# Performance work log

Hardware: AMD Instinct MI355X
Metric: run time of the kernel (lower is better)

Reference implementation:

```python
import jax, jax.numpy as jnp
import numpy as np

B, VN, LN = 32, 576, 128
V_DIM, L_DIM, E, H = 1024, 768, 1024, 16
D = E // H
SCALE = H ** -0.5  # note: original scales by num_heads**-0.5, NOT head_dim**-0.5


def _xavier(key, shape):
    fan_in, fan_out = shape[1], shape[0]
    lim = np.sqrt(6.0 / (fan_in + fan_out))
    return jax.random.uniform(key, shape, jnp.float32, -lim, lim)


def setup_inputs() -> dict:
    key = jax.random.key(0)
    ks = jax.random.split(key, 10)
    return {
        "v": jax.random.normal(ks[0], (B, VN, V_DIM), jnp.float32),
        "l": jax.random.normal(ks[1], (B, LN, L_DIM), jnp.float32),
        "attention_mask_l": jnp.zeros((LN,), jnp.float32),
        "Wvq": _xavier(ks[2], (E, V_DIM)), "bvq": jnp.zeros((E,), jnp.float32),
        "Wlk": _xavier(ks[3], (E, L_DIM)), "blk": jnp.zeros((E,), jnp.float32),
        "Wvv": _xavier(ks[4], (E, V_DIM)), "bvv": jnp.zeros((E,), jnp.float32),
        "Wlv": _xavier(ks[5], (E, L_DIM)), "blv": jnp.zeros((E,), jnp.float32),
        "Wvo": _xavier(ks[6], (V_DIM, E)), "bvo": jnp.zeros((V_DIM,), jnp.float32),
        "Wlo": _xavier(ks[7], (L_DIM, E)), "blo": jnp.zeros((L_DIM,), jnp.float32),
    }


def reference(v, l, attention_mask_l, Wvq, bvq, Wlk, blk, Wvv, bvv, Wlv, blv, Wvo, bvo, Wlo, blo):
    # mode='vl'; dropout is identity (eval mode)
    q = (v @ Wvq.T + bvq).reshape(B, VN, H, D)          # vision queries
    k = (l @ Wlk.T + blk).reshape(B, LN, H, D)          # language keys
    vv = (v @ Wvv.T + bvv).reshape(B, VN, H, D)         # vision values
    lv = (l @ Wlv.T + blv).reshape(B, LN, H, D)         # language values

    attn = jnp.einsum('bqhd,bkhd->bhqk', q, k) * SCALE   # [B,H,vN,lN]
    attn_v = attn + attention_mask_l[None, None, None, :]
    attn_v = jax.nn.softmax(attn_v, axis=-1)             # softmax over lN
    attn_l = jax.nn.softmax(attn, axis=-2)               # transposed softmax over vN

    xl = jnp.einsum('bhqk,bqhd->bkhd', attn_l, vv).reshape(B, LN, E)
    xv = jnp.einsum('bhqk,bkhd->bqhd', attn_v, lv).reshape(B, VN, E)

    xl = xl @ Wlo.T + blo
    xv = xv @ Wvo.T + bvo
    return xv, xl
```

## Files before the change

kernel.cpp:

```cpp
#include <hip/hip_runtime.h>
#include <stdint.h>


typedef unsigned short bfu;
typedef __attribute__((ext_vector_type(4))) float f32x4;
typedef __attribute__((ext_vector_type(8))) short short8;
typedef __attribute__((ext_vector_type(4))) unsigned short u16x4;

#define MFMA16(a,b,c) __builtin_amdgcn_mfma_f32_16x16x32_bf16((a),(b),(c),0,0,0)
#define SCALE_QK 0.25f

__device__ __forceinline__ unsigned short f2bf(float x) {
  unsigned int u = __float_as_uint(x);
  u += 0x7fffu + ((u >> 16) & 1u);
  return (unsigned short)(u >> 16);
}

__device__ __forceinline__ void gload_lds16(const void* g, void* l) {
  __builtin_amdgcn_global_load_lds(
      reinterpret_cast<__attribute__((address_space(1))) void*>(
          reinterpret_cast<uintptr_t>(g)),
      reinterpret_cast<__attribute__((address_space(3))) void*>(
          (uint32_t)reinterpret_cast<uintptr_t>(l)),
      16, 0, 0);
}

__global__ void cvt_f32_bf16(const float* __restrict__ x, bfu* __restrict__ y, int n4) {
  for (int i = blockIdx.x * blockDim.x + threadIdx.x; i < n4; i += gridDim.x * blockDim.x) {
    const float4 f = *reinterpret_cast<const float4*>(x + (size_t)i * 4);
    u16x4 o;
    o[0] = f2bf(f.x); o[1] = f2bf(f.y); o[2] = f2bf(f.z); o[3] = f2bf(f.w);
    *reinterpret_cast<u16x4*>(y + (size_t)i * 4) = o;
  }
}

struct CvtArgs {
  const float* src[7];
  bfu* dst[7];
  int n4[7];
};

__global__ void cvt_multi(CvtArgs a) {
  const int s = blockIdx.y;
  const float* __restrict__ x = a.src[s];
  bfu* __restrict__ y = a.dst[s];
  const int n4 = a.n4[s];
  for (int i = blockIdx.x * blockDim.x + threadIdx.x; i < n4; i += gridDim.x * blockDim.x) {
    const float4 f = *reinterpret_cast<const float4*>(x + (size_t)i * 4);
    u16x4 o;
    o[0] = f2bf(f.x); o[1] = f2bf(f.y); o[2] = f2bf(f.z); o[3] = f2bf(f.w);
    *reinterpret_cast<u16x4*>(y + (size_t)i * 4) = o;
  }
}

__global__ __launch_bounds__(256) void gemm_bt(
    const bfu* __restrict__ A, const bfu* __restrict__ W, const float* __restrict__ bias,
    bfu* __restrict__ Cb, float* __restrict__ Cf, bfu* __restrict__ Ct, int R, int colsplit,
    int ldc, int M, int N, int K, int nbn)
{
  __shared__ bfu As[128 * 32];
  __shared__ bfu Bs[128 * 32];
  const int nbm = M >> 7;
  const int bid = blockIdx.x;
  int bm, bn;
  if ((nbm & 7) == 0) {
    const int xcd = bid & 7, j = bid >> 3;
    const int jm = j / nbn;
    bm = xcd * (nbm >> 3) + jm;
    bn = j - jm * nbn;
  } else { bm = bid / nbn; bn = bid - (bid / nbn) * nbn; }

  const int t = threadIdx.x, l = t & 63, w = t >> 6;
  const int g = l >> 4, c = l & 15;
  const int wr = (w >> 1) * 64, wc = (w & 1) * 64;

  f32x4 zero = {0.f, 0.f, 0.f, 0.f};
  f32x4 acc[4][4];
  for (int m = 0; m < 4; ++m)
    for (int n = 0; n < 4; ++n) acc[m][n] = zero;

  const int rowA = l >> 2;
  const int kb   = (l & 3) * 16;

  for (int k0 = 0; k0 < K; k0 += 32) {
#pragma unroll
    for (int i = 0; i < 2; ++i) {
      int chunk = w * 2 + i;
      int r = chunk * 16 + rowA;
      const char* ga = (const char*)(A + (size_t)(bm * 128 + r) * K + k0) + kb;
      const char* gb = (const char*)(W + (size_t)(bn * 128 + r) * K + k0) + kb;
      gload_lds16(ga, (char*)As + chunk * 1024);
      gload_lds16(gb, (char*)Bs + chunk * 1024);
    }
    __syncthreads();
    short8 a[4], bf[4];
#pragma unroll
    for (int m = 0; m < 4; ++m)
      a[m] = *reinterpret_cast<const short8*>(&As[(wr + m * 16 + c) * 32 + g * 8]);
#pragma unroll
    for (int n = 0; n < 4; ++n)
      bf[n] = *reinterpret_cast<const short8*>(&Bs[(wc + n * 16 + c) * 32 + g * 8]);
#pragma unroll
    for (int m = 0; m < 4; ++m)
#pragma unroll
      for (int n = 0; n < 4; ++n)
        acc[m][n] = MFMA16(a[m], bf[n], acc[m][n]);
    __syncthreads();
  }

#pragma unroll
  for (int n = 0; n < 4; ++n) {
    const int col = bn * 128 + wc + n * 16 + c;
    const float bs = bias[col];
    if (col >= colsplit) {
      const int colp = col - colsplit;
      const int hh = colp >> 6, dd = colp & 63;
#pragma unroll
      for (int m = 0; m < 4; ++m) {
        const int row0 = bm * 128 + wr + m * 16 + g * 4;
        const int bb = row0 / R, q0 = row0 - bb * R;
        u16x4 pk;
#pragma unroll
        for (int r = 0; r < 4; ++r) pk[r] = f2bf(acc[m][n][r] + bs);
        *reinterpret_cast<u16x4*>(Ct + ((size_t)(bb * 16 + hh) * 64 + dd) * R + q0) = pk;
      }
    } else {
#pragma unroll
      for (int m = 0; m < 4; ++m) {
        const int row0 = bm * 128 + wr + m * 16 + g * 4;
#pragma unroll
        for (int r = 0; r < 4; ++r) {
          float val = acc[m][n][r] + bs;
          size_t idx = (size_t)(row0 + r) * ldc + col;
          if (Cf) Cf[idx] = val;
          else    Cb[idx] = f2bf(val);
        }
      }
    }
  }
}

template<int RT>
__global__ __launch_bounds__(512, 2) void gemm288(
    const bfu* __restrict__ A, const bfu* __restrict__ W, const float* __restrict__ bias,
    bfu* __restrict__ Cb, float* __restrict__ Cf, bfu* __restrict__ Ct, int colsplit,
    int ldc, int M, int N, int K, int nbn)
{
  __shared__ bfu lds[2 * 36864];

  const int tid = threadIdx.x;
  const int w = tid >> 6, lane = tid & 63;
  const int g = lane >> 4, c = lane & 15;
  const int wr = w >> 2, wc = w & 3;
  const int rb0 = wr ? 208 : 0;
  const int rb1 = wr ? 144 : 80;

  const int nbm = M / 288;
  int bm, bn;
  { const int xcd = blockIdx.x & 7, j = blockIdx.x >> 3;
    const int jm = j / nbn; bm = xcd * (nbm >> 3) + jm; bn = j - jm * nbn; }

  const int nt = K >> 6;

  const int srow8 = lane >> 3;
  const int sslot = lane & 7;
  const int swzE  = ((sslot * 16) ^ (srow8 << 4)) >> 1;
  const bfu* srcA = A + (size_t)(bm * 288 + 8 * w + srow8) * K + swzE;
  const bfu* srcB = W + (size_t)(bn * 256 + 8 * w + srow8) * K + swzE;

#define AB(cur) (lds + (cur) * 36864)
#define BB(cur) (lds + (cur) * 36864 + 20480)
#define STAGE_A(cur, j, k0) gload_lds16(srcA + (size_t)(64 * (j)) * K + (k0), \
    (void*)(AB(cur) + (64 * (j) + 8 * w) * 64))
#define STAGE_B(cur, j, k0) gload_lds16(srcB + (size_t)(64 * (j)) * K + (k0), \
    (void*)(BB(cur) + (64 * (j) + 8 * w) * 64))

  short8 aF[5][2], bF[4][2];
  const int swzR = ((c & 7) << 3);

#define LDA(cur, mh, CNT) { _Pragma("unroll") for (int mi2 = 0; mi2 < (CNT); ++mi2) \
    _Pragma("unroll") for (int ks = 0; ks < 2; ++ks) \
      aF[mi2][ks] = *reinterpret_cast<const short8*>( \
        AB(cur) + (((mh) ? rb1 : rb0) + mi2 * 16 + c) * 64 + ((ks * 32 + g * 8) ^ swzR)); }
#define LDB(cur, nh) { _Pragma("unroll") for (int ni2 = 0; ni2 < 2; ++ni2) \
    _Pragma("unroll") for (int ks = 0; ks < 2; ++ks) \
      bF[(nh) * 2 + ni2][ks] = *reinterpret_cast<const short8*>( \
        BB(cur) + (wc * 64 + (nh) * 32 + ni2 * 16 + c) * 64 + ((ks * 32 + g * 8) ^ swzR)); }

  f32x4 acc[9][4];
  const f32x4 zero = {0.f, 0.f, 0.f, 0.f};
#pragma unroll
  for (int mi = 0; mi < 9; ++mi)
#pragma unroll
    for (int ni = 0; ni < 4; ++ni) acc[mi][ni] = zero;

#define PH_MFMA(mh, nh, CNT) { __builtin_amdgcn_s_setprio(1); \
    _Pragma("unroll") for (int mi2 = 0; mi2 < (CNT); ++mi2) \
    _Pragma("unroll") for (int ni2 = 0; ni2 < 2; ++ni2) \
    _Pragma("unroll") for (int ks = 0; ks < 2; ++ks) \
      acc[(mh) * 5 + mi2][(nh) * 2 + ni2] = \
        MFMA16(aF[mi2][ks], bF[(nh) * 2 + ni2][ks], acc[(mh) * 5 + mi2][(nh) * 2 + ni2]); \
    __builtin_amdgcn_s_setprio(0); }

  STAGE_B(0, 0, 0); STAGE_B(0, 1, 0); STAGE_B(0, 2, 0); STAGE_B(0, 3, 0);
  STAGE_A(0, 0, 0); STAGE_A(0, 1, 0); STAGE_A(0, 3, 0); STAGE_A(0, 4, 0); STAGE_A(0, 2, 0);
  asm volatile("s_waitcnt vmcnt(0)" ::: "memory");
  __builtin_amdgcn_s_barrier();

  int cur = 0;
  for (int t = 0; t < nt - 1; ++t) {
    const int k1 = (t + 1) * 64;
    LDB(cur, 0); LDA(cur, 0, 5);
    STAGE_B(cur ^ 1, 0, k1); STAGE_B(cur ^ 1, 1, k1);
    STAGE_B(cur ^ 1, 2, k1); STAGE_B(cur ^ 1, 3, k1);
    __builtin_amdgcn_s_barrier();
    PH_MFMA(0, 0, 5);
    __builtin_amdgcn_s_barrier();
    LDB(cur, 1);
    STAGE_A(cur ^ 1, 0, k1); STAGE_A(cur ^ 1, 1, k1);
    STAGE_A(cur ^ 1, 3, k1); STAGE_A(cur ^ 1, 4, k1);
    asm volatile("s_waitcnt vmcnt(8)" ::: "memory");
    __builtin_amdgcn_s_barrier();
    PH_MFMA(0, 1, 5);
    __builtin_amdgcn_s_barrier();
    LDA(cur, 1, 4);
    STAGE_A(cur ^ 1, 2, k1);
    __builtin_amdgcn_s_barrier();
    PH_MFMA(1, 0, 4);
    __builtin_amdgcn_s_barrier();
    asm volatile("s_waitcnt vmcnt(1)" ::: "memory");
    __builtin_amdgcn_s_barrier();
    PH_MFMA(1, 1, 4);
    __builtin_amdgcn_s_barrier();
    cur ^= 1;
  }
  LDB(cur, 0); LDA(cur, 0, 5);
  __builtin_amdgcn_s_barrier();
  PH_MFMA(0, 0, 5);
  __builtin_amdgcn_s_barrier();
  LDB(cur, 1);
  asm volatile("s_waitcnt vmcnt(0)" ::: "memory");
  __builtin_amdgcn_s_barrier();
  PH_MFMA(0, 1, 5);
  __builtin_amdgcn_s_barrier();
  LDA(cur, 1, 4);
  PH_MFMA(1, 0, 4);
  PH_MFMA(1, 1, 4);

  const bool isCt = (RT > 0) && (bn * 256 >= colsplit);

  if (isCt) {
    const int RTl = (RT > 0 ? RT : 1);
    short* bw = (short*)lds + w * 2432;
#pragma unroll
    for (int ni = 0; ni < 4; ++ni) {
      const float bs = bias[bn * 256 + wc * 64 + ni * 16 + c];
#pragma unroll
      for (int mh = 0; mh < 2; ++mh)
#pragma unroll
        for (int mi2 = 0; mi2 < 5; ++mi2) {
          if (mh == 1 && mi2 == 4) continue;
          const int qlb = wr ? (mh ? 0 : 64) : (mh ? 80 : 0);
          u16x4 pk;
#pragma unroll
          for (int r = 0; r < 4; ++r) pk[r] = f2bf(acc[mh * 5 + mi2][ni][r] + bs);
          *reinterpret_cast<u16x4*>(&bw[c * 152 + qlb + mi2 * 16 + g * 4]) = pk;
        }
#pragma unroll
      for (int it = 0; it < 5; ++it) {
        const int idx = it * 64 + lane;
        if (idx < 288) {
          const int dd = idx / 18, q8 = idx - dd * 18;
          short8 vx = *reinterpret_cast<const short8*>(&bw[dd * 152 + q8 * 8]);
          const int colp = bn * 256 + wc * 64 + ni * 16 + dd - colsplit;
          const int hh = colp >> 6, dl = colp & 63;
          const int qg = bm * 288 + wr * 144 + q8 * 8;
          const int bb = qg / RTl, q0 = qg - bb * RTl;
          *reinterpret_cast<short8*>(Ct + ((size_t)(bb * 16 + hh) * 64 + dl) * RTl + q0) = vx;
        }
      }
    }
  } else if (Cf) {
#pragma unroll
    for (int ni = 0; ni < 4; ++ni) {
      const int col = bn * 256 + wc * 64 + ni * 16 + c;
      const float bs = bias[col];
#pragma unroll
      for (int mh = 0; mh < 2; ++mh)
#pragma unroll
        for (int mi2 = 0; mi2 < 5; ++mi2) {
          if (mh == 1 && mi2 == 4) continue;
          const int row0 = bm * 288 + (mh ? rb1 : rb0) + mi2 * 16 + g * 4;
#pragma unroll
          for (int r = 0; r < 4; ++r)
            Cf[(size_t)(row0 + r) * ldc + col] = acc[mh * 5 + mi2][ni][r] + bs;
        }
    }
  } else {
    short* bw = (short*)lds + w * 1216;
    float bs4[4];
#pragma unroll
    for (int ni = 0; ni < 4; ++ni) bs4[ni] = bias[bn * 256 + wc * 64 + ni * 16 + c];
#pragma unroll
    for (int mh = 0; mh < 2; ++mh)
#pragma unroll
      for (int mi2 = 0; mi2 < 5; ++mi2) {
        if (mh == 1 && mi2 == 4) continue;
#pragma unroll
        for (int ni = 0; ni < 4; ++ni)
#pragma unroll
          for (int r = 0; r < 4; ++r)
            bw[(g * 4 + r) * 72 + ni * 16 + c] = (short)f2bf(acc[mh * 5 + mi2][ni][r] + bs4[ni]);
#pragma unroll
        for (int half = 0; half < 2; ++half) {
          const int rr = (lane >> 3) + half * 8;
          const int cc2 = (lane & 7) * 8;
          short8 vx = *reinterpret_cast<const short8*>(&bw[rr * 72 + cc2]);
          const int grow = bm * 288 + (mh ? rb1 : rb0) + mi2 * 16 + rr;
          *reinterpret_cast<short8*>(Cb + (size_t)grow * ldc + bn * 256 + wc * 64 + cc2) = vx;
        }
      }
  }
#undef AB
#undef BB
#undef STAGE_A
#undef STAGE_B
#undef LDA
#undef LDB
#undef PH_MFMA
}

__device__ __forceinline__ int pvt_off(int q, int kbyte) { return q * 256 + (kbyte ^ ((q & 7) << 4)); }

__global__ __launch_bounds__(256) void attn_xv(
    const bfu* __restrict__ Q, const bfu* __restrict__ Kl,
    const bfu* __restrict__ LVt, const float* __restrict__ mask,
    bfu* __restrict__ xv, bfu* __restrict__ PT, float* __restrict__ colpart)
{
  __shared__ short Ks[128 * 64];
  __shared__ short LVs[64 * 128];
  __shared__ short PvT[4][2048];

  const int blk = blockIdx.x;
  const int bh = blk & 511, qc = blk >> 9;
  const int b = bh >> 4, h = bh & 15;
  const int t = threadIdx.x, l = t & 63, w = t >> 6;
  const int g = l >> 4, c = l & 15;
  const int qt = qc * 4 + w;

  const bfu* Qp  = Q   + ((size_t)b * 576 * 1024 + h * 64);
  const bfu* Kp  = Kl  + ((size_t)b * 128 * 1024 + h * 64);
  const bfu* LVp = LVt + (size_t)bh * 64 * 128;
  const f32x4 zero = {0.f, 0.f, 0.f, 0.f};

  {
    const int kr = l >> 3;
    const bfu* sK = Kp + (size_t)(w * 8 + kr) * 1024 + (((l & 7) ^ kr) * 8);
#pragma unroll
    for (int i = 0; i < 4; ++i)
      gload_lds16(sK + (size_t)(i * 32) * 1024, (void*)&Ks[(i * 32 + w * 8) * 64]);
    const int lr = l >> 4;
    const int key = (w * 4 + lr) & 7;
    const bfu* sLV = LVp + (size_t)(w * 4 + lr) * 128 + ((l >> 3) & 1) * 64 + (((l & 7) ^ key) * 8);
#pragma unroll
    for (int i = 0; i < 4; ++i)
      gload_lds16(sLV + (size_t)(i * 16) * 128, (void*)&LVs[(i * 16 + w * 4) * 128]);
  }
  float mk[8];
#pragma unroll
  for (int kt = 0; kt < 8; ++kt) mk[kt] = mask[kt * 16 + c];
  __syncthreads();

  f32x4 sacc[8];
#pragma unroll
  for (int kt = 0; kt < 8; ++kt) sacc[kt] = zero;
  __builtin_amdgcn_s_setprio(1);
#pragma unroll
  for (int kk = 0; kk < 2; ++kk) {
    short8 aq = *reinterpret_cast<const short8*>(Qp + (size_t)(qt * 16 + c) * 1024 + kk * 32 + g * 8);
#pragma unroll
    for (int kt = 0; kt < 8; ++kt) {
      short8 bk = *reinterpret_cast<const short8*>(
          &Ks[(kt * 16 + c) * 64 + (((kk * 4 + g) ^ (c & 7)) * 8)]);
      sacc[kt] = MFMA16(aq, bk, sacc[kt]);
    }
  }
  __builtin_amdgcn_s_setprio(0);

  char* myPv = (char*)&PvT[w][0];
  float rs[4] = {0, 0, 0, 0};
  float colacc[8];
#pragma unroll
  for (int kt = 0; kt < 8; ++kt) {
    u16x4 pk;
    float ca = 0.f;
#pragma unroll
    for (int r = 0; r < 4; ++r) {
      float Ev = __expf(fmaf(sacc[kt][r], SCALE_QK, mk[kt]));
      rs[r] += Ev;
      ca += Ev;
      pk[r] = f2bf(Ev);
      *reinterpret_cast<unsigned short*>(myPv + pvt_off(g * 4 + r, 2 * (kt * 16 + c))) = pk[r];
    }
    colacc[kt] = ca;
    *reinterpret_cast<u16x4*>(PT + ((size_t)bh * 128 + kt * 16 + c) * 576 + qt * 16 + g * 4) = pk;
  }
#pragma unroll
  for (int r = 0; r < 4; ++r) {
    rs[r] += __shfl_xor(rs[r], 1);
    rs[r] += __shfl_xor(rs[r], 2);
    rs[r] += __shfl_xor(rs[r], 4);
    rs[r] += __shfl_xor(rs[r], 8);
  }

  short8 av[4];
#pragma unroll
  for (int kc = 0; kc < 4; ++kc)
    av[kc] = *reinterpret_cast<const short8*>(myPv + pvt_off(c, kc * 64 + g * 16));
  f32x4 oxv[4];
#pragma unroll
  for (int dt = 0; dt < 4; ++dt) oxv[dt] = zero;
  __builtin_amdgcn_s_setprio(1);
#pragma unroll
  for (int dt = 0; dt < 4; ++dt)
#pragma unroll
    for (int kc = 0; kc < 4; ++kc) {
      short8 bv = *reinterpret_cast<const short8*>(
          &LVs[(dt * 16 + c) * 128 + (kc >> 1) * 64 + ((((kc & 1) * 4 + g) ^ (c & 7)) * 8)]);
      oxv[dt] = MFMA16(av[kc], bv, oxv[dt]);
    }
  __builtin_amdgcn_s_setprio(0);
#pragma unroll
  for (int r = 0; r < 4; ++r) rs[r] = 1.0f / rs[r];

  short* bw = (short*)&PvT[w][0];
#pragma unroll
  for (int dt = 0; dt < 4; ++dt)
#pragma unroll
    for (int r = 0; r < 4; ++r)
      bw[(g * 4 + r) * 72 + dt * 16 + c] = (short)f2bf(oxv[dt][r] * rs[r]);
#pragma unroll
  for (int half = 0; half < 2; ++half) {
    const int rr = (l >> 3) + half * 8;
    const int cc = (l & 7) * 8;
    short8 vx = *reinterpret_cast<const short8*>(&bw[rr * 72 + cc]);
    *reinterpret_cast<short8*>(xv + (size_t)(b * 576 + qt * 16 + rr) * 1024 + h * 64 + cc) = vx;
  }

#pragma unroll
  for (int kt = 0; kt < 8; ++kt) {
    colacc[kt] += __shfl_xor(colacc[kt], 16);
    colacc[kt] += __shfl_xor(colacc[kt], 32);
  }
  if (g == 0) {
#pragma unroll
    for (int kt = 0; kt < 8; ++kt)
      colpart[(size_t)(bh * 36 + qt) * 128 + kt * 16 + c] = colacc[kt];
  }
}

__global__ __launch_bounds__(64) void attn_xl(
    const bfu* __restrict__ PT, const bfu* __restrict__ VVt,
    const float* __restrict__ colpart, bfu* __restrict__ xl)
{
  __shared__ short XL[1168];

  const int blk = blockIdx.x;
  const int bh = blk & 511, kt = blk >> 9;
  const int b = bh >> 4, h = bh & 15;
  const int l = threadIdx.x;
  const int g = l >> 4, c = l & 15;

  const bfu* PTb  = PT  + ((size_t)bh * 128 + kt * 16 + c) * 576;
  const bfu* VVp  = VVt + (size_t)bh * 64 * 576;
  const f32x4 zero = {0.f, 0.f, 0.f, 0.f};

  float s = 0.f;
  const float* cp = colpart + (size_t)bh * 36 * 128 + kt * 16 + c;
#pragma unroll
  for (int qc = 0; qc < 36; ++qc) s += cp[qc * 128];
  float sinv = 1.0f / s;
  float ci[4];
#pragma unroll
  for (int r = 0; r < 4; ++r) ci[r] = __shfl(sinv, g * 4 + r);

  f32x4 acc[4];
#pragma unroll
  for (int dt = 0; dt < 4; ++dt) acc[dt] = zero;

  __builtin_amdgcn_s_setprio(1);
  for (int p = 0; p < 18; ++p) {
    short8 ap = *reinterpret_cast<const short8*>(PTb + p * 32 + g * 8);
#pragma unroll
    for (int dt = 0; dt < 4; ++dt) {
      short8 bv = *reinterpret_cast<const short8*>(VVp + (size_t)(dt * 16 + c) * 576 + p * 32 + g * 8);
      acc[dt] = MFMA16(ap, bv, acc[dt]);
    }
  }
  __builtin_amdgcn_s_setprio(0);

#pragma unroll
  for (int dt = 0; dt < 4; ++dt)
#pragma unroll
    for (int r = 0; r < 4; ++r)
      XL[(g * 4 + r) * 72 + dt * 16 + c] = (short)f2bf(acc[dt][r] * ci[r]);
#pragma unroll
  for (int half = 0; half < 2; ++half) {
    const int rr = (l >> 3) + half * 8;
    const int cc = (l & 7) * 8;
    short8 vx = *reinterpret_cast<const short8*>(&XL[rr * 72 + cc]);
    *reinterpret_cast<short8*>(xl + (size_t)(b * 128 + kt * 16 + rr) * 1024 + h * 64 + cc) = vx;
  }
}

static inline int cvt_grid(int n4) {
  int g = (n4 + 255) / 256;
  return g > 4096 ? 4096 : g;
}

extern "C" void kernel_launch(void* const* d_in, const int* in_sizes, int n_in,
                              void* d_out, int out_size, void* d_ws, size_t ws_size,
                              hipStream_t stream)
{
  const float* v    = (const float*)d_in[0];
  const float* lx   = (const float*)d_in[1];
  const float* mask = (const float*)d_in[2];
  const float* Wvq  = (const float*)d_in[3];
  const float* bvq  = (const float*)d_in[4];
  const float* Wlk  = (const float*)d_in[5];
  const float* blk  = (const float*)d_in[6];
  const float* Wvv  = (const float*)d_in[7];
  const float* bvv  = (const float*)d_in[8];
  const float* Wlv  = (const float*)d_in[9];
  const float* blv  = (const float*)d_in[10];
  const float* Wvo  = (const float*)d_in[11];
  const float* bvo  = (const float*)d_in[12];
  const float* Wlo  = (const float*)d_in[13];
  const float* blo  = (const float*)d_in[14];

  float* out_xv = (float*)d_out;
  float* out_xl = out_xv + (size_t)18432 * 1024;

  bfu* ws   = (bfu*)d_ws;
  bfu* vb   = ws;
  bfu* lb   = vb   + 18874368;
  bfu* wqv  = lb   + 3145728;
  bfu* wklv = wqv  + 2097152;
  bfu* wvo  = wklv + 1572864;
  bfu* wlo  = wvo  + 1048576;
  bfu* Qb   = wlo  + 786432;
  bfu* VVt  = Qb   + 18874368;
  bfu* Kb   = VVt  + 18874368;
  bfu* LVt  = Kb   + 4194304;
  bfu* PT   = LVt  + 4194304;
  float* biasqv = (float*)(PT + 37748736);
  float* biaskl = biasqv + 2048;
  float* colpart = (float*)lb;

  cvt_f32_bf16<<<cvt_grid(18874368 / 4), 256, 0, stream>>>(v, vb, 18874368 / 4);
  CvtArgs ca;
  ca.src[0] = lx;  ca.dst[0] = lb;             ca.n4[0] = 3145728 / 4;
  ca.src[1] = Wvq; ca.dst[1] = wqv;            ca.n4[1] = 1048576 / 4;
  ca.src[2] = Wvv; ca.dst[2] = wqv + 1048576;  ca.n4[2] = 1048576 / 4;
  ca.src[3] = Wlk; ca.dst[3] = wklv;           ca.n4[3] = 786432 / 4;
  ca.src[4] = Wlv; ca.dst[4] = wklv + 786432;  ca.n4[4] = 786432 / 4;
  ca.src[5] = Wvo; ca.dst[5] = wvo;            ca.n4[5] = 1048576 / 4;
  ca.src[6] = Wlo; ca.dst[6] = wlo;            ca.n4[6] = 786432 / 4;
  cvt_multi<<<dim3(1024, 7), 256, 0, stream>>>(ca);
  hipMemcpyAsync(biasqv,        bvq, 1024 * sizeof(float), hipMemcpyDeviceToDevice, stream);
  hipMemcpyAsync(biasqv + 1024, bvv, 1024 * sizeof(float), hipMemcpyDeviceToDevice, stream);
  hipMemcpyAsync(biaskl,        blk, 1024 * sizeof(float), hipMemcpyDeviceToDevice, stream);
  hipMemcpyAsync(biaskl + 1024, blv, 1024 * sizeof(float), hipMemcpyDeviceToDevice, stream);

  gemm288<576><<<64 * 8, 512, 0, stream>>>(vb, wqv, biasqv, Qb, nullptr, VVt, 1024, 1024,
                                           18432, 2048, 1024, 8);
  gemm_bt<<<32 * 16, 256, 0, stream>>>(lb, wklv, biaskl, Kb, nullptr, LVt, 128, 1024, 1024,
                                       4096, 2048, 768, 16);

  attn_xv<<<512 * 9, 256, 0, stream>>>(Qb, Kb, LVt, mask, vb, PT, colpart);
  attn_xl<<<512 * 8, 64, 0, stream>>>(PT, VVt, colpart, Kb);

  gemm288<0><<<64 * 4, 512, 0, stream>>>(vb, wvo, bvo, nullptr, out_xv, nullptr, 1 << 30, 1024,
                                         18432, 1024, 1024, 4);
  gemm_bt<<<32 * 6, 256, 0, stream>>>(Kb, wlo, blo, nullptr, out_xl, nullptr, 0, 768, 768,
                                      4096, 768, 1024, 6);
}
```

Measured before the change: 313.5 us.

## Fuse vision and language attention into one per-head kernel, dropping the PT buffer

Merges attn_xv and attn_xl into a single attn_bi kernel with one block per (batch, head). Each block loops over nine query chunks and accumulates the transposed attention-times-vision-values product from the probability tiles already held in LDS. This removes the global write and re-read of the large bf16 probability buffer and the column-sum partials. It cuts the grid from thousands of blocks to 512 and serialises the query loop, which lowers parallelism and adds barriers. It also replaces four bias memcpys with one small kernel and stages the fp32 GEMM epilogue through LDS so the output stores are coalesced vector stores.

```diff
diff --git a/kernel.cpp b/kernel.cpp
--- a/kernel.cpp
+++ b/kernel.cpp
@@ -51,6 +51,21 @@
     o[0] = f2bf(f.x); o[1] = f2bf(f.y); o[2] = f2bf(f.z); o[3] = f2bf(f.w);
     *reinterpret_cast<u16x4*>(y + (size_t)i * 4) = o;
   }
+}
+
+__global__ void bias_concat(const float* __restrict__ a, const float* __restrict__ b,
+                            const float* __restrict__ c2, const float* __restrict__ d,
+                            float* __restrict__ qv, float* __restrict__ kl) {
+  const int i = threadIdx.x * 4;
+  const float4* s;
+  float* o;
+  switch (blockIdx.x) {
+    case 0: s = (const float4*)a;  o = qv;        break;
+    case 1: s = (const float4*)b;  o = qv + 1024; break;
+    case 2: s = (const float4*)c2; o = kl;        break;
+    default: s = (const float4*)d; o = kl + 1024; break;
+  }
+  *reinterpret_cast<float4*>(o + i) = s[threadIdx.x];
 }
 
 __global__ __launch_bounds__(256) void gemm_bt(
@@ -281,21 +296,29 @@
       }
     }
   } else if (Cf) {
-#pragma unroll
-    for (int ni = 0; ni < 4; ++ni) {
-      const int col = bn * 256 + wc * 64 + ni * 16 + c;
-      const float bs = bias[col];
-#pragma unroll
-      for (int mh = 0; mh < 2; ++mh)
-#pragma unroll
-        for (int mi2 = 0; mi2 < 5; ++mi2) {
-          if (mh == 1 && mi2 == 4) continue;
-          const int row0 = bm * 288 + (mh ? rb1 : rb0) + mi2 * 16 + g * 4;
+    float* bwf = (float*)lds + w * 1088;
+    float bs4[4];
+#pragma unroll
+    for (int ni = 0; ni < 4; ++ni) bs4[ni] = bias[bn * 256 + wc * 64 + ni * 16 + c];
+#pragma unroll
+    for (int mh = 0; mh < 2; ++mh)
+#pragma unroll
+      for (int mi2 = 0; mi2 < 5; ++mi2) {
+        if (mh == 1 && mi2 == 4) continue;
+#pragma unroll
+        for (int ni = 0; ni < 4; ++ni)
 #pragma unroll
           for (int r = 0; r < 4; ++r)
-            Cf[(size_t)(row0 + r) * ldc + col] = acc[mh * 5 + mi2][ni][r] + bs;
+            bwf[(g * 4 + r) * 68 + ni * 16 + c] = acc[mh * 5 + mi2][ni][r] + bs4[ni];
+#pragma unroll
+        for (int p = 0; p < 4; ++p) {
+          const int rr = lane >> 2;
+          const int ch = p * 4 + (lane & 3);
+          f32x4 vx = *reinterpret_cast<const f32x4*>(&bwf[rr * 68 + ch * 4]);
+          const int row = bm * 288 + (mh ? rb1 : rb0) + mi2 * 16 + rr;
+          *reinterpret_cast<f32x4*>(Cf + (size_t)row * ldc + bn * 256 + wc * 64 + ch * 4) = vx;
         }
-    }
+      }
   } else {
     short* bw = (short*)lds + w * 1216;
     float bs4[4];
@@ -332,25 +355,26 @@
 
 __device__ __forceinline__ int pvt_off(int q, int kbyte) { return q * 256 + (kbyte ^ ((q & 7) << 4)); }
 
-__global__ __launch_bounds__(256) void attn_xv(
+__global__ __launch_bounds__(256) void attn_bi(
     const bfu* __restrict__ Q, const bfu* __restrict__ Kl,
-    const bfu* __restrict__ LVt, const float* __restrict__ mask,
-    bfu* __restrict__ xv, bfu* __restrict__ PT, float* __restrict__ colpart)
+    const bfu* __restrict__ LVt, const bfu* __restrict__ VVt,
+    const float* __restrict__ mask,
+    bfu* __restrict__ xv, bfu* __restrict__ xl)
 {
   __shared__ short Ks[128 * 64];
   __shared__ short LVs[64 * 128];
   __shared__ short PvT[4][2048];
-
-  const int blk = blockIdx.x;
-  const int bh = blk & 511, qc = blk >> 9;
+  __shared__ float cpart[4][128];
+
+  const int bh = blockIdx.x;
   const int b = bh >> 4, h = bh & 15;
   const int t = threadIdx.x, l = t & 63, w = t >> 6;
   const int g = l >> 4, c = l & 15;
-  const int qt = qc * 4 + w;
 
   const bfu* Qp  = Q   + ((size_t)b * 576 * 1024 + h * 64);
   const bfu* Kp  = Kl  + ((size_t)b * 128 * 1024 + h * 64);
   const bfu* LVp = LVt + (size_t)bh * 64 * 128;
+  const bfu* VVp = VVt + (size_t)bh * 64 * 576;
   const f32x4 zero = {0.f, 0.f, 0.f, 0.f};
 
   {
@@ -371,80 +395,118 @@
   for (int kt = 0; kt < 8; ++kt) mk[kt] = mask[kt * 16 + c];
   __syncthreads();
 
-  f32x4 sacc[8];
-#pragma unroll
-  for (int kt = 0; kt < 8; ++kt) sacc[kt] = zero;
-  __builtin_amdgcn_s_setprio(1);
-#pragma unroll
-  for (int kk = 0; kk < 2; ++kk) {
-    short8 aq = *reinterpret_cast<const short8*>(Qp + (size_t)(qt * 16 + c) * 1024 + kk * 32 + g * 8);
+  char* myPv = (char*)&PvT[w][0];
+  float colacc[8] = {0, 0, 0, 0, 0, 0, 0, 0};
+  f32x4 xlacc[2][4];
+#pragma unroll
+  for (int kt2 = 0; kt2 < 2; ++kt2)
+#pragma unroll
+    for (int dt = 0; dt < 4; ++dt) xlacc[kt2][dt] = zero;
+
+  for (int it = 0; it < 9; ++it) {
+    const int qt = it * 4 + w;
+    f32x4 sacc[8];
+#pragma unroll
+    for (int kt = 0; kt < 8; ++kt) sacc[kt] = zero;
+    __builtin_amdgcn_s_setprio(1);
+#pragma unroll
+    for (int kk = 0; kk < 2; ++kk) {
+      short8 aq = *reinterpret_cast<const short8*>(Qp + (size_t)(qt * 16 + c) * 1024 + kk * 32 + g * 8);
+#pragma unroll
+      for (int kt = 0; kt < 8; ++kt) {
+        short8 bk = *reinterpret_cast<const short8*>(
+            &Ks[(kt * 16 + c) * 64 + (((kk * 4 + g) ^ (c & 7)) * 8)]);
+        sacc[kt] = MFMA16(aq, bk, sacc[kt]);
+      }
+    }
+    __builtin_amdgcn_s_setprio(0);
+
+    float rs[4] = {0, 0, 0, 0};
 #pragma unroll
     for (int kt = 0; kt < 8; ++kt) {
-      short8 bk = *reinterpret_cast<const short8*>(
-          &Ks[(kt * 16 + c) * 64 + (((kk * 4 + g) ^ (c & 7)) * 8)]);
-      sacc[kt] = MFMA16(aq, bk, sacc[kt]);
-    }
-  }
-  __builtin_amdgcn_s_setprio(0);
-
-  char* myPv = (char*)&PvT[w][0];
-  float rs[4] = {0, 0, 0, 0};
-  float colacc[8];
-#pragma unroll
-  for (int kt = 0; kt < 8; ++kt) {
-    u16x4 pk;
-    float ca = 0.f;
+      float ca = 0.f;
+#pragma unroll
+      for (int r = 0; r < 4; ++r) {
+        float Ev = __expf(fmaf(sacc[kt][r], SCALE_QK, mk[kt]));
+        rs[r] += Ev;
+        ca += Ev;
+        *reinterpret_cast<unsigned short*>(myPv + pvt_off(g * 4 + r, 2 * (kt * 16 + c))) = f2bf(Ev);
+      }
+      colacc[kt] += ca;
+    }
 #pragma unroll
     for (int r = 0; r < 4; ++r) {
-      float Ev = __expf(fmaf(sacc[kt][r], SCALE_QK, mk[kt]));
-      rs[r] += Ev;
-      ca += Ev;
-      pk[r] = f2bf(Ev);
-      *reinterpret_cast<unsigned short*>(myPv + pvt_off(g * 4 + r, 2 * (kt * 16 + c))) = pk[r];
-    }
-    colacc[kt] = ca;
-    *reinterpret_cast<u16x4*>(PT + ((size_t)bh * 128 + kt * 16 + c) * 576 + qt * 16 + g * 4) = pk;
-  }
-#pragma unroll
-  for (int r = 0; r < 4; ++r) {
-    rs[r] += __shfl_xor(rs[r], 1);
-    rs[r] += __shfl_xor(rs[r], 2);
-    rs[r] += __shfl_xor(rs[r], 4);
-    rs[r] += __shfl_xor(rs[r], 8);
-  }
-
-  short8 av[4];
-#pragma unroll
-  for (int kc = 0; kc < 4; ++kc)
-    av[kc] = *reinterpret_cast<const short8*>(myPv + pvt_off(c, kc * 64 + g * 16));
-  f32x4 oxv[4];
-#pragma unroll
-  for (int dt = 0; dt < 4; ++dt) oxv[dt] = zero;
-  __builtin_amdgcn_s_setprio(1);
-#pragma unroll
-  for (int dt = 0; dt < 4; ++dt)
-#pragma unroll
-    for (int kc = 0; kc < 4; ++kc) {
-      short8 bv = *reinterpret_cast<const short8*>(
-          &LVs[(dt * 16 + c) * 128 + (kc >> 1) * 64 + ((((kc & 1) * 4 + g) ^ (c & 7)) * 8)]);
-      oxv[dt] = MFMA16(av[kc], bv, oxv[dt]);
-    }
-  __builtin_amdgcn_s_setprio(0);
-#pragma unroll
-  for (int r = 0; r < 4; ++r) rs[r] = 1.0f / rs[r];
-
-  short* bw = (short*)&PvT[w][0];
-#pragma unroll
-  for (int dt = 0; dt < 4; ++dt)
-#pragma unroll
-    for (int r = 0; r < 4; ++r)
-      bw[(g * 4 + r) * 72 + dt * 16 + c] = (short)f2bf(oxv[dt][r] * rs[r]);
-#pragma unroll
-  for (int half = 0; half < 2; ++half) {
-    const int rr = (l >> 3) + half * 8;
-    const int cc = (l & 7) * 8;
-    short8 vx = *reinterpret_cast<const short8*>(&bw[rr * 72 + cc]);
-    *reinterpret_cast<short8*>(xv + (size_t)(b * 576 + qt * 16 + rr) * 1024 + h * 64 + cc) = vx;
+      rs[r] += __shfl_xor(rs[r], 1);
+      rs[r] += __shfl_xor(rs[r], 2);
+      rs[r] += __shfl_xor(rs[r], 4);
+      rs[r] += __shfl_xor(rs[r], 8);
+    }
+
+    short8 av[4];
+#pragma unroll
+    for (int kc = 0; kc < 4; ++kc)
+      av[kc] = *reinterpret_cast<const short8*>(myPv + pvt_off(c, kc * 64 + g * 16));
+    f32x4 oxv[4];
+#pragma unroll
+    for (int dt = 0; dt < 4; ++dt) oxv[dt] = zero;
+    __builtin_amdgcn_s_setprio(1);
+#pragma unroll
+    for (int dt = 0; dt < 4; ++dt)
+#pragma unroll
+      for (int kc = 0; kc < 4; ++kc) {
+        short8 bv = *reinterpret_cast<const short8*>(
+            &LVs[(dt * 16 + c) * 128 + (kc >> 1) * 64 + ((((kc & 1) * 4 + g) ^ (c & 7)) * 8)]);
+        oxv[dt] = MFMA16(av[kc], bv, oxv[dt]);
+      }
+    __builtin_amdgcn_s_setprio(0);
+#pragma unroll
+    for (int r = 0; r < 4; ++r) rs[r] = 1.0f / rs[r];
+
+    __syncthreads();
+
+#pragma unroll
+    for (int kt2 = 0; kt2 < 2; ++kt2) {
+      const int kbyte = 2 * (w * 32 + kt2 * 16 + c);
+      short8 ap[2];
+#pragma unroll
+      for (int ks = 0; ks < 2; ++ks) {
+        const int wq = ks * 2 + (g >> 1);
+        const int qb8 = (g & 1) * 8;
+        const char* tile = (const char*)&PvT[wq][0];
+#pragma unroll
+        for (int j = 0; j < 8; ++j) {
+          const int ql = qb8 + j;
+          ap[ks][j] = *reinterpret_cast<const short*>(
+              tile + ql * 256 + (kbyte ^ (j << 4)));
+        }
+      }
+      __builtin_amdgcn_s_setprio(1);
+#pragma unroll
+      for (int dt = 0; dt < 4; ++dt) {
+#pragma unroll
+        for (int ks = 0; ks < 2; ++ks) {
+          short8 bv = *reinterpret_cast<const short8*>(
+              VVp + (size_t)(dt * 16 + c) * 576 + it * 64 + ks * 32 + g * 8);
+          xlacc[kt2][dt] = MFMA16(ap[ks], bv, xlacc[kt2][dt]);
+        }
+      }
+      __builtin_amdgcn_s_setprio(0);
+    }
+    __syncthreads();
+
+    short* bw = (short*)&PvT[w][0];
+#pragma unroll
+    for (int dt = 0; dt < 4; ++dt)
+#pragma unroll
+      for (int r = 0; r < 4; ++r)
+        bw[(g * 4 + r) * 72 + dt * 16 + c] = (short)f2bf(oxv[dt][r] * rs[r]);
+#pragma unroll
+    for (int half = 0; half < 2; ++half) {
+      const int rr = (l >> 3) + half * 8;
+      const int cc = (l & 7) * 8;
+      short8 vx = *reinterpret_cast<const short8*>(&bw[rr * 72 + cc]);
+      *reinterpret_cast<short8*>(xv + (size_t)(b * 576 + qt * 16 + rr) * 1024 + h * 64 + cc) = vx;
+    }
   }
 
 #pragma unroll
@@ -454,62 +516,31 @@
   }
   if (g == 0) {
 #pragma unroll
-    for (int kt = 0; kt < 8; ++kt)
-      colpart[(size_t)(bh * 36 + qt) * 128 + kt * 16 + c] = colacc[kt];
-  }
-}
-
-__global__ __launch_bounds__(64) void attn_xl(
-    const bfu* __restrict__ PT, const bfu* __restrict__ VVt,
-    const float* __restrict__ colpart, bfu* __restrict__ xl)
-{
-  __shared__ short XL[1168];
-
-  const int blk = blockIdx.x;
-  const int bh = blk & 511, kt = blk >> 9;
-  const int b = bh >> 4, h = bh & 15;
-  const int l = threadIdx.x;
-  const int g = l >> 4, c = l & 15;
-
-  const bfu* PTb  = PT  + ((size_t)bh * 128 + kt * 16 + c) * 576;
-  const bfu* VVp  = VVt + (size_t)bh * 64 * 576;
-  const f32x4 zero = {0.f, 0.f, 0.f, 0.f};
-
-  float s = 0.f;
-  const float* cp = colpart + (size_t)bh * 36 * 128 + kt * 16 + c;
-#pragma unroll
-  for (int qc = 0; qc < 36; ++qc) s += cp[qc * 128];
-  float sinv = 1.0f / s;
-  float ci[4];
-#pragma unroll
-  for (int r = 0; r < 4; ++r) ci[r] = __shfl(sinv, g * 4 + r);
-
-  f32x4 acc[4];
-#pragma unroll
-  for (int dt = 0; dt < 4; ++dt) acc[dt] = zero;
-
-  __builtin_amdgcn_s_setprio(1);
-  for (int p = 0; p < 18; ++p) {
-    short8 ap = *reinterpret_cast<const short8*>(PTb + p * 32 + g * 8);
-#pragma unroll
-    for (int dt = 0; dt < 4; ++dt) {
-      short8 bv = *reinterpret_cast<const short8*>(VVp + (size_t)(dt * 16 + c) * 576 + p * 32 + g * 8);
-      acc[dt] = MFMA16(ap, bv, acc[dt]);
-    }
-  }
-  __builtin_amdgcn_s_setprio(0);
-
-#pragma unroll
-  for (int dt = 0; dt < 4; ++dt)
-#pragma unroll
-    for (int r = 0; r < 4; ++r)
-      XL[(g * 4 + r) * 72 + dt * 16 + c] = (short)f2bf(acc[dt][r] * ci[r]);
-#pragma unroll
-  for (int half = 0; half < 2; ++half) {
-    const int rr = (l >> 3) + half * 8;
-    const int cc = (l & 7) * 8;
-    short8 vx = *reinterpret_cast<const short8*>(&XL[rr * 72 + cc]);
-    *reinterpret_cast<short8*>(xl + (size_t)(b * 128 + kt * 16 + rr) * 1024 + h * 64 + cc) = vx;
+    for (int kt = 0; kt < 8; ++kt) cpart[w][kt * 16 + c] = colacc[kt];
+  }
+  __syncthreads();
+
+  short* bw = (short*)&PvT[w][0];
+#pragma unroll
+  for (int kt2 = 0; kt2 < 2; ++kt2) {
+    float ci[4];
+#pragma unroll
+    for (int r = 0; r < 4; ++r) {
+      const int k = w * 32 + kt2 * 16 + g * 4 + r;
+      ci[r] = 1.0f / (cpart[0][k] + cpart[1][k] + cpart[2][k] + cpart[3][k]);
+    }
+#pragma unroll
+    for (int dt = 0; dt < 4; ++dt)
+#pragma unroll
+      for (int r = 0; r < 4; ++r)
+        bw[(g * 4 + r) * 72 + dt * 16 + c] = (short)f2bf(xlacc[kt2][dt][r] * ci[r]);
+#pragma unroll
+    for (int half = 0; half < 2; ++half) {
+      const int rr = (l >> 3) + half * 8;
+      const int cc = (l & 7) * 8;
+      short8 vx = *reinterpret_cast<const short8*>(&bw[rr * 72 + cc]);
+      *reinterpret_cast<short8*>(xl + (size_t)(b * 128 + w * 32 + kt2 * 16 + rr) * 1024 + h * 64 + cc) = vx;
+    }
   }
 }
 
@@ -552,10 +583,8 @@
   bfu* VVt  = Qb   + 18874368;
   bfu* Kb   = VVt  + 18874368;
   bfu* LVt  = Kb   + 4194304;
-  bfu* PT   = LVt  + 4194304;
-  float* biasqv = (float*)(PT + 37748736);
+  float* biasqv = (float*)(LVt + 4194304);
   float* biaskl = biasqv + 2048;
-  float* colpart = (float*)lb;
 
   cvt_f32_bf16<<<cvt_grid(18874368 / 4), 256, 0, stream>>>(v, vb, 18874368 / 4);
   CvtArgs ca;
@@ -567,18 +596,14 @@
   ca.src[5] = Wvo; ca.dst[5] = wvo;            ca.n4[5] = 1048576 / 4;
   ca.src[6] = Wlo; ca.dst[6] = wlo;            ca.n4[6] = 786432 / 4;
   cvt_multi<<<dim3(1024, 7), 256, 0, stream>>>(ca);
-  hipMemcpyAsync(biasqv,        bvq, 1024 * sizeof(float), hipMemcpyDeviceToDevice, stream);
-  hipMemcpyAsync(biasqv + 1024, bvv, 1024 * sizeof(float), hipMemcpyDeviceToDevice, stream);
-  hipMemcpyAsync(biaskl,        blk, 1024 * sizeof(float), hipMemcpyDeviceToDevice, stream);
-  hipMemcpyAsync(biaskl + 1024, blv, 1024 * sizeof(float), hipMemcpyDeviceToDevice, stream);
+  bias_concat<<<4, 256, 0, stream>>>(bvq, bvv, blk, blv, biasqv, biaskl);
 
   gemm288<576><<<64 * 8, 512, 0, stream>>>(vb, wqv, biasqv, Qb, nullptr, VVt, 1024, 1024,
                                            18432, 2048, 1024, 8);
   gemm_bt<<<32 * 16, 256, 0, stream>>>(lb, wklv, biaskl, Kb, nullptr, LVt, 128, 1024, 1024,
                                        4096, 2048, 768, 16);
 
-  attn_xv<<<512 * 9, 256, 0, stream>>>(Qb, Kb, LVt, mask, vb, PT, colpart);
-  attn_xl<<<512 * 8, 64, 0, stream>>>(PT, VVt, colpart, Kb);
+  attn_bi<<<512, 256, 0, stream>>>(Qb, Kb, LVt, VVt, mask, vb, Kb);
 
   gemm288<0><<<64 * 4, 512, 0, stream>>>(vb, wvo, bvo, nullptr, out_xv, nullptr, 1 << 30, 1024,
                                          18432, 1024, 1024, 4);
```

Measured after the change: 256.5 us. 18.2% less time.
